# Kernel optimization log

Measured on AMD Instinct MI355X. Metric: run time of the kernel, lower is better.

The kernel has to match this reference:

```python
import jax, jax.numpy as jnp
import numpy as np

C = 64           # channels
CPG = 8          # channel_per_group
G = C // CPG     # offset groups = 8
K = 27           # 3x3x3 taps
N, D, H, W = 2, 8, 56, 56


def conv3d(x, w, b=None):
    y = jax.lax.conv_general_dilated(
        x, w, window_strides=(1, 1, 1), padding=[(1, 1)] * 3,
        dimension_numbers=('NCDHW', 'OIDHW', 'NCDHW'))
    if b is not None:
        y = y + b.reshape(1, -1, 1, 1, 1)
    return y


def deform_conv3d(x, off, w, groups):
    # x: [N,C,D,H,W]; off: [N, G*3*27, D,H,W]; w: [O,C,3,3,3]
    n, cin, d, h, wd = x.shape
    cpg = cin // groups
    p = d * h * wd
    off = off.reshape(n, groups, K, 3, d, h, wd)
    # kernel tap displacements in (kd,kh,kw) order, each in {-1,0,1}
    r = jnp.arange(3, dtype=x.dtype) - 1.0
    taps = jnp.stack(jnp.meshgrid(r, r, r, indexing='ij'), axis=-1).reshape(K, 3)
    gd = jnp.arange(d, dtype=x.dtype)[:, None, None]
    gh = jnp.arange(h, dtype=x.dtype)[None, :, None]
    gw = jnp.arange(wd, dtype=x.dtype)[None, None, :]
    # sampling positions [N,G,K,D,H,W]
    pd = gd + taps[:, 0][:, None, None, None] + off[:, :, :, 0]
    ph = gh + taps[:, 1][:, None, None, None] + off[:, :, :, 1]
    pw = gw + taps[:, 2][:, None, None, None] + off[:, :, :, 2]
    d0 = jnp.floor(pd); h0 = jnp.floor(ph); w0 = jnp.floor(pw)
    fd, fh, fw = pd - d0, ph - h0, pw - w0
    d0 = d0.astype(jnp.int32); h0 = h0.astype(jnp.int32); w0 = w0.astype(jnp.int32)
    xflat = x.reshape(n, groups, cpg, p)[:, :, None]  # [N,G,1,Cpg,P]
    acc = jnp.zeros((n, groups, K, cpg, p), x.dtype)
    for cd in (0, 1):
        for ch in (0, 1):
            for cw in (0, 1):
                idd, idh, idw = d0 + cd, h0 + ch, w0 + cw
                wgt = ((fd if cd else 1.0 - fd)
                       * (fh if ch else 1.0 - fh)
                       * (fw if cw else 1.0 - fw))
                valid = ((idd >= 0) & (idd < d) & (idh >= 0) & (idh < h)
                         & (idw >= 0) & (idw < wd)).astype(x.dtype)
                lin = ((jnp.clip(idd, 0, d - 1) * h + jnp.clip(idh, 0, h - 1)) * wd
                       + jnp.clip(idw, 0, wd - 1))
                g = jnp.take_along_axis(xflat, lin.reshape(n, groups, K, 1, p), axis=-1)
                acc = acc + g * (wgt * valid).reshape(n, groups, K, 1, p)
    # [N,G,K,Cpg,P] -> [N,K,C,P]
    vals = acc.transpose(0, 2, 1, 3, 4).reshape(n, K, cin, p)
    out = jnp.einsum('oik,nkip->nop', w.reshape(w.shape[0], cin, K), vals)
    return out.reshape(n, -1, d, h, wd)


def batchnorm(x, gamma, beta, eps=1e-5):
    m = x.mean((0, 2, 3, 4), keepdims=True)
    v = x.var((0, 2, 3, 4), keepdims=True)
    return (gamma.reshape(1, -1, 1, 1, 1) * (x - m) * jax.lax.rsqrt(v + eps)
            + beta.reshape(1, -1, 1, 1, 1))


def setup_inputs() -> dict:
    key = jax.random.key(0)
    ks = jax.random.split(key, 4)
    fan = C * K
    x = jax.random.normal(ks[0], (N, C, D, H, W), jnp.float32)
    w_off = jax.random.normal(ks[1], (G * 3 * K, C, 3, 3, 3), jnp.float32) * 0.01
    b_off = jnp.zeros((G * 3 * K,), jnp.float32)
    w1 = jax.random.normal(ks[2], (C, C, 3, 3, 3), jnp.float32) / np.sqrt(fan).astype(np.float32)
    w2 = jax.random.normal(ks[3], (C, C, 3, 3, 3), jnp.float32) / np.sqrt(fan).astype(np.float32)
    return dict(x=x, w_off=w_off, b_off=b_off, w1=w1,
                gamma1=jnp.ones((C,), jnp.float32), beta1=jnp.zeros((C,), jnp.float32),
                w2=w2, b2=jnp.zeros((C,), jnp.float32),
                gamma2=jnp.ones((C,), jnp.float32), beta2=jnp.zeros((C,), jnp.float32))


def reference(x, w_off, b_off, w1, gamma1, beta1, w2, b2, gamma2, beta2):
    residual = x
    off = conv3d(x, w_off, b_off)
    out = deform_conv3d(x, off, w1, G)
    out = jax.nn.relu(batchnorm(out, gamma1, beta1))
    out = conv3d(out, w2, b2)
    out = batchnorm(out, gamma2, beta2) + residual
    return jax.nn.relu(out)
```

## Files before the change

### kernel.cpp

```cpp
#include <hip/hip_runtime.h>
#include <hip/hip_bf16.h>

#define N_ 2
#define C_ 64
#define D_ 8
#define H_ 56
#define W_ 56
#define HW_ (H_*W_)
#define P_ (D_*HW_)
#define G_ 8
#define CPG_ 8
#define K_ 27
#define CO_OFF_ 648
#define MP_ 768
#define KK_ 1728
#define KB_ (KK_*2)

typedef __attribute__((ext_vector_type(8))) short shortx8;
typedef __attribute__((ext_vector_type(4))) float floatx4;
#define AS1 __attribute__((address_space(1)))
#define AS3 __attribute__((address_space(3)))

__device__ inline float b2f(unsigned short u) {
    union { unsigned u; float f; } x; x.u = ((unsigned)u) << 16; return x.f;
}
__device__ inline unsigned short f2b(float f) {
    union { float f; unsigned u; } x; x.f = f;
    unsigned r = (x.u + 0x7fffu + ((x.u >> 16) & 1u)) >> 16;
    return (unsigned short)r;
}
__device__ inline float lof(unsigned u) { union { unsigned u; float f; } x; x.u = u << 16; return x.f; }
__device__ inline float hif(unsigned u) { union { unsigned u; float f; } x; x.u = u & 0xffff0000u; return x.f; }
__device__ inline unsigned cvt_pk_bf16(float a, float b) {
    unsigned r;
    asm("v_cvt_pk_bf16_f32 %0, %1, %2" : "=v"(r) : "v"(a), "v"(b));
    return r;
}


__global__ __launch_bounds__(256) void transpose_xt_kernel(
    const float* __restrict__ x, unsigned short* __restrict__ xt)
{
    __shared__ unsigned short tile[64][65];
    int b  = blockIdx.x;
    int n  = b / (P_/64);
    int p0 = (b % (P_/64))*64;
    int tid = threadIdx.x;
    int j  = tid & 63;
    int c0 = (tid >> 6)*16;
    for (int r = 0; r < 16; ++r)
        tile[c0 + r][j] = f2b(x[((size_t)n*C_ + c0 + r)*P_ + p0 + j]);
    __syncthreads();
    unsigned* dst = (unsigned*)(xt + ((size_t)n*P_ + p0)*C_);
    #pragma unroll
    for (int it = 0; it < 8; ++it) {
        int wi  = it*256 + tid;
        int row = wi >> 5;
        int c   = (wi & 31)*2;
        unsigned lo = tile[c][row], hi = tile[c+1][row];
        dst[(size_t)row*32 + (wi & 31)] = lo | (hi << 16);
    }
}

__global__ __launch_bounds__(256) void permA1k_kernel(
    const float* __restrict__ w, unsigned short* __restrict__ A)
{
    int i = blockIdx.x*256 + threadIdx.x;
    if (i >= MP_*KK_) return;
    int m = i / KK_, r = i % KK_;
    int kk = r / 64, ci = r % 64;
    A[i] = (m < CO_OFF_) ? f2b(w[((size_t)m*C_ + ci)*K_ + kk]) : (unsigned short)0;
}

__global__ __launch_bounds__(256) void perm_w_kernel(
    const float* __restrict__ w, unsigned short* __restrict__ At)
{
    int tid = blockIdx.x*256 + threadIdx.x;
    if (tid >= C_*KK_) return;
    int o  = tid / KK_;
    int r  = tid % KK_;
    int k  = r / 64, i = r % 64;
    At[tid] = f2b(w[((size_t)o*C_ + i)*K_ + k]);
}

__global__ __launch_bounds__(256, 2) void conv_off_fused(
    const unsigned short* __restrict__ A,
    const unsigned short* __restrict__ xt,
    const float* __restrict__ bias,
    unsigned short* __restrict__ off2)
{
    __shared__ __align__(16) short As[2][16*512];
    __shared__ __align__(16) short Bs[32*512];
    int tid = threadIdx.x;
    int w = tid >> 6, lane = tid & 63;
    int n   = blockIdx.x / 490;
    int bid = blockIdx.x % 490;
    int mt = bid / 98, nt = bid % 98;
    int m0 = mt*128, p0 = nt*256;
    int lm = lane & 15, lq = lane >> 4;

    const unsigned short* xtn = xt + (size_t)n*P_*C_;
    unsigned short* out2 = off2 + (size_t)n*216*P_*3;

    const char* Ab0 = (const char*)A + (size_t)(m0 + w*32 + lm)*KB_ + lq*16;
    const char* Ab1 = Ab0 + (size_t)16*KB_;

    int oct = lane & 7;
    int prj[8], dj[8], hj[8], wj[8];
    #pragma unroll
    for (int j = 0; j < 8; ++j) {
        int prow = j*32 + w*8 + (lane >> 3);
        prj[j] = prow;
        int p = p0 + prow;
        dj[j] = p / HW_;
        int hw2 = p % HW_;
        hj[j] = hw2 / W_;
        wj[j] = hw2 % W_;
    }

    auto stageA = [&](int kt, int buf) {
        __builtin_amdgcn_global_load_lds((const AS1 unsigned*)(Ab0 + kt*128),      (AS3 unsigned*)(&As[buf][(w*2)*512]),     16, 0, 0);
        __builtin_amdgcn_global_load_lds((const AS1 unsigned*)(Ab1 + kt*128),      (AS3 unsigned*)(&As[buf][(w*2+1)*512]),   16, 0, 0);
        __builtin_amdgcn_global_load_lds((const AS1 unsigned*)(Ab0 + kt*128 + 64), (AS3 unsigned*)(&As[buf][(8+w*2)*512]),   16, 0, 0);
        __builtin_amdgcn_global_load_lds((const AS1 unsigned*)(Ab1 + kt*128 + 64), (AS3 unsigned*)(&As[buf][(8+w*2+1)*512]), 16, 0, 0);
    };
    auto loadB = [&](int kt, uint4* B) {
        int kd = kt/9 - 1, kh = (kt/3)%3 - 1, kw = kt%3 - 1;
        int delta = kd*HW_ + kh*W_ + kw;
        #pragma unroll
        for (int j = 0; j < 8; ++j) {
            bool v = ((unsigned)(dj[j]+kd) < (unsigned)D_) &&
                     ((unsigned)(hj[j]+kh) < (unsigned)H_) &&
                     ((unsigned)(wj[j]+kw) < (unsigned)W_);
            uint4 val = {0u,0u,0u,0u};
            if (v) val = *(const uint4*)(xtn + (size_t)(p0 + prj[j] + delta)*C_ + oct*8);
            B[j] = val;
        }
    };

    int mh = w >> 1, nh = w & 1;
    floatx4 acc[4][8];
    #pragma unroll
    for (int i = 0; i < 4; ++i)
        #pragma unroll
        for (int j = 0; j < 8; ++j)
            acc[i][j] = (floatx4){0.f, 0.f, 0.f, 0.f};

    uint4 Bcur[8], Bnext[8];
    #pragma unroll
    for (int j = 0; j < 8; ++j) Bnext[j] = (uint4){0u,0u,0u,0u};
    stageA(0, 0);
    loadB(0, Bcur);

    for (int kt = 0; kt < 27; ++kt) {
        int buf = kt & 1;
        __syncthreads();
        #pragma unroll
        for (int j = 0; j < 8; ++j) {
            int chunk = (oct>>2)*16 + (prj[j]>>4);
            *(uint4*)&Bs[chunk*512 + ((oct&3)*16 + ((prj[j]&15) ^ oct))*8] = Bcur[j];
        }
        __syncthreads();
        if (kt < 26) { stageA(kt+1, buf^1); loadB(kt+1, Bnext); }
        #pragma unroll
        for (int ks = 0; ks < 2; ++ks) {
            int swzB = (lq*16 + (lm ^ (ks*4 + lq)))*8;
            shortx8 a[4];
            #pragma unroll
            for (int i = 0; i < 4; ++i) a[i] = *(const shortx8*)&As[buf][(ks*8 + 4*mh + i)*512 + lane*8];
            #pragma unroll
            for (int j = 0; j < 8; ++j) {
                shortx8 b = *(const shortx8*)&Bs[(ks*16 + 8*nh + j)*512 + swzB];
                #pragma unroll
                for (int i = 0; i < 4; ++i)
                    acc[i][j] = __builtin_amdgcn_mfma_f32_16x16x32_bf16(a[i], b, acc[i][j], 0, 0, 0);
            }
        }
        #pragma unroll
        for (int j = 0; j < 8; ++j) Bcur[j] = Bnext[j];
    }

    #pragma unroll
    for (int i = 0; i < 4; ++i) {
        int cob = m0 + (4*mh+i)*16 + lq*4;
        #pragma unroll
        for (int r = 0; r < 4; ++r) {
            int co = cob + r;
            float bv = bias[co];
            int row2 = co / 3, comp = co % 3;
            size_t base = (size_t)row2*P_*3 + comp;
            #pragma unroll
            for (int j = 0; j < 8; ++j) {
                int col = p0 + (8*nh+j)*16 + lm;
                out2[base + (size_t)col*3] = f2b(acc[i][j][r] + bv);
            }
        }
    }
}

__global__ __launch_bounds__(256) void conv_off_tail(
    const unsigned short* __restrict__ A,
    const unsigned short* __restrict__ xt,
    const float* __restrict__ bias,
    unsigned short* __restrict__ off2)
{
    __shared__ __align__(16) short As[54*512];
    __shared__ __align__(16) short Bs[16*512];
    int tid = threadIdx.x;
    int w = tid >> 6, lane = tid & 63;
    int n  = blockIdx.x / 196;
    int p0 = (blockIdx.x % 196)*128;
    int lm = lane & 15, lq = lane >> 4;

    const unsigned short* xtn = xt + (size_t)n*P_*C_;
    unsigned short* out2 = off2 + (size_t)n*216*P_*3;

    const char* Abase = (const char*)A + (size_t)(640 + lm)*KB_ + lq*16;
    for (int ch = w; ch < 54; ch += 4)
        __builtin_amdgcn_global_load_lds((const AS1 unsigned*)(Abase + ch*64),
                                         (AS3 unsigned*)(As + ch*512), 16, 0, 0);

    int oct = lane & 7;
    int prj[4], dj[4], hj[4], wj[4];
    #pragma unroll
    for (int j = 0; j < 4; ++j) {
        int prow = j*32 + w*8 + (lane >> 3);
        prj[j] = prow;
        int p = p0 + prow;
        dj[j] = p / HW_;
        int hw2 = p % HW_;
        hj[j] = hw2 / W_;
        wj[j] = hw2 % W_;
    }
    auto loadB = [&](int kt, uint4* B) {
        int kd = kt/9 - 1, kh = (kt/3)%3 - 1, kw = kt%3 - 1;
        int delta = kd*HW_ + kh*W_ + kw;
        #pragma unroll
        for (int j = 0; j < 4; ++j) {
            bool v = ((unsigned)(dj[j]+kd) < (unsigned)D_) &&
                     ((unsigned)(hj[j]+kh) < (unsigned)H_) &&
                     ((unsigned)(wj[j]+kw) < (unsigned)W_);
            uint4 val = {0u,0u,0u,0u};
            if (v) val = *(const uint4*)(xtn + (size_t)(p0 + prj[j] + delta)*C_ + oct*8);
            B[j] = val;
        }
    };

    floatx4 acc[2];
    acc[0] = (floatx4){0.f,0.f,0.f,0.f};
    acc[1] = (floatx4){0.f,0.f,0.f,0.f};

    uint4 Bcur[4], Bnext[4];
    #pragma unroll
    for (int j = 0; j < 4; ++j) Bnext[j] = (uint4){0u,0u,0u,0u};
    loadB(0, Bcur);

    for (int kt = 0; kt < 27; ++kt) {
        __syncthreads();
        #pragma unroll
        for (int j = 0; j < 4; ++j) {
            int chunk = (oct>>2)*8 + (prj[j]>>4);
            *(uint4*)&Bs[chunk*512 + ((oct&3)*16 + ((prj[j]&15) ^ oct))*8] = Bcur[j];
        }
        __syncthreads();
        if (kt < 26) loadB(kt+1, Bnext);
        #pragma unroll
        for (int ks = 0; ks < 2; ++ks) {
            int swzB = (lq*16 + (lm ^ (ks*4 + lq)))*8;
            shortx8 a = *(const shortx8*)&As[(kt*2 + ks)*512 + lane*8];
            #pragma unroll
            for (int j = 0; j < 2; ++j) {
                shortx8 b = *(const shortx8*)&Bs[(ks*8 + w*2 + j)*512 + swzB];
                acc[j] = __builtin_amdgcn_mfma_f32_16x16x32_bf16(a, b, acc[j], 0, 0, 0);
            }
        }
        #pragma unroll
        for (int j = 0; j < 4; ++j) Bcur[j] = Bnext[j];
    }

    #pragma unroll
    for (int j = 0; j < 2; ++j) {
        #pragma unroll
        for (int r = 0; r < 4; ++r) {
            int co = 640 + lq*4 + r;
            if (co < CO_OFF_) {
                int col = p0 + w*32 + j*16 + lm;
                out2[((size_t)(co/3)*P_ + col)*3 + (co%3)] = f2b(acc[j][r] + bias[co]);
            }
        }
    }
}

__global__ __launch_bounds__(256) void deform_fused(
    const unsigned short* __restrict__ xt,
    const unsigned short* __restrict__ off2,
    const unsigned short* __restrict__ A,
    unsigned short* __restrict__ y1t)
{
    __shared__ __align__(16) short SH[12288];
    int tid = threadIdx.x;
    int w = tid >> 6, lane = tid & 63;
    int n  = blockIdx.x / (P_/32);
    int p0 = (blockIdx.x % (P_/32))*32;
    int lm = lane & 15, lq = lane >> 4;

    const unsigned short* offn = off2 + (size_t)n*216*P_*3;
    const uint4* xg0 = (const uint4*)(xt + (size_t)n*P_*C_);

    const char* Ab = (const char*)A + (size_t)(w*16 + lm)*KB_ + lq*16;

    int g = lane & 7;
    int prow = tid >> 3;
    int p = p0 + prow;
    int dd = p / HW_;
    int hw2 = p % HW_;
    int hh = hw2 / W_;
    int ww = hw2 % W_;
    int bchunk = (g>>2)*2 + (prow>>4);
    int boffs  = ((g&3)*16 + ((prow&15) ^ g))*8;

    auto stageA = [&](int kt, int buf) {
        __builtin_amdgcn_global_load_lds((const AS1 unsigned*)(Ab + kt*128),      (AS3 unsigned*)(SH + buf*4096 + w*512),     16, 0, 0);
        __builtin_amdgcn_global_load_lds((const AS1 unsigned*)(Ab + kt*128 + 64), (AS3 unsigned*)(SH + buf*4096 + (4+w)*512), 16, 0, 0);
    };
    auto loadOff = [&](int kt, float* o) {
        size_t idx = ((size_t)(g*K_ + kt)*P_ + p)*3;
        o[0] = b2f(offn[idx]);
        o[1] = b2f(offn[idx + 1]);
        o[2] = b2f(offn[idx + 2]);
    };
    auto issueCorners = [&](int kt, float* o, uint4* V, float* Wt) {
        int kd = kt/9 - 1, kh = (kt/3)%3 - 1, kw = kt%3 - 1;
        float pd = (float)(dd + kd) + o[0];
        float ph = (float)(hh + kh) + o[1];
        float pw = (float)(ww + kw) + o[2];
        float fd0 = floorf(pd), fh0 = floorf(ph), fw0 = floorf(pw);
        int d0 = (int)fd0, h0 = (int)fh0, w0i = (int)fw0;
        float fd = pd - fd0, fh = ph - fh0, fw = pw - fw0;
        int dc0 = min(max(d0, 0), D_-1),   dc1 = min(max(d0+1, 0), D_-1);
        int hc0 = min(max(h0, 0), H_-1),   hc1 = min(max(h0+1, 0), H_-1);
        int wc0 = min(max(w0i, 0), W_-1),  wc1 = min(max(w0i+1, 0), W_-1);
        float wd0 = ((unsigned)d0      < (unsigned)D_) ? 1.f - fd : 0.f;
        float wd1 = ((unsigned)(d0+1)  < (unsigned)D_) ? fd       : 0.f;
        float wh0 = ((unsigned)h0      < (unsigned)H_) ? 1.f - fh : 0.f;
        float wh1 = ((unsigned)(h0+1)  < (unsigned)H_) ? fh       : 0.f;
        float ww0 = ((unsigned)w0i     < (unsigned)W_) ? 1.f - fw : 0.f;
        float ww1 = ((unsigned)(w0i+1) < (unsigned)W_) ? fw       : 0.f;
        int rb00 = (dc0*H_ + hc0)*W_, rb01 = (dc0*H_ + hc1)*W_;
        int rb10 = (dc1*H_ + hc0)*W_, rb11 = (dc1*H_ + hc1)*W_;
        float wdh00 = wd0*wh0, wdh01 = wd0*wh1, wdh10 = wd1*wh0, wdh11 = wd1*wh1;
        V[0] = xg0[(size_t)(rb00+wc0)*8 + g];  Wt[0] = wdh00*ww0;
        V[1] = xg0[(size_t)(rb00+wc1)*8 + g];  Wt[1] = wdh00*ww1;
        V[2] = xg0[(size_t)(rb01+wc0)*8 + g];  Wt[2] = wdh01*ww0;
        V[3] = xg0[(size_t)(rb01+wc1)*8 + g];  Wt[3] = wdh01*ww1;
        V[4] = xg0[(size_t)(rb10+wc0)*8 + g];  Wt[4] = wdh10*ww0;
        V[5] = xg0[(size_t)(rb10+wc1)*8 + g];  Wt[5] = wdh10*ww1;
        V[6] = xg0[(size_t)(rb11+wc0)*8 + g];  Wt[6] = wdh11*ww0;
        V[7] = xg0[(size_t)(rb11+wc1)*8 + g];  Wt[7] = wdh11*ww1;
    };
    auto reduceCorners = [&](uint4* V, float* Wt, uint4& o4) {
        float res[CPG_];
        #pragma unroll
        for (int c = 0; c < CPG_; ++c) res[c] = 0.f;
        #pragma unroll
        for (int c = 0; c < 8; ++c) {
            uint4 v4 = V[c];
            float wgt = Wt[c];
            res[0] = fmaf(wgt, lof(v4.x), res[0]);
            res[1] = fmaf(wgt, hif(v4.x), res[1]);
            res[2] = fmaf(wgt, lof(v4.y), res[2]);
            res[3] = fmaf(wgt, hif(v4.y), res[3]);
            res[4] = fmaf(wgt, lof(v4.z), res[4]);
            res[5] = fmaf(wgt, hif(v4.z), res[5]);
            res[6] = fmaf(wgt, lof(v4.w), res[6]);
            res[7] = fmaf(wgt, hif(v4.w), res[7]);
        }
        o4.x = cvt_pk_bf16(res[0], res[1]);
        o4.y = cvt_pk_bf16(res[2], res[3]);
        o4.z = cvt_pk_bf16(res[4], res[5]);
        o4.w = cvt_pk_bf16(res[6], res[7]);
    };

    int mh = w >> 1, nh = w & 1;
    floatx4 acc[2];
    acc[0] = (floatx4){0.f,0.f,0.f,0.f};
    acc[1] = (floatx4){0.f,0.f,0.f,0.f};

    float offA[3], offB[3], offT[3];
    uint4 Vv[8]; float Wt[8];
    uint4 o4cur;

    stageA(0, 0);
    loadOff(0, offA);
    loadOff(1, offB);
    issueCorners(0, offA, Vv, Wt);
    reduceCorners(Vv, Wt, o4cur);
    *(uint4*)&SH[8192 + bchunk*512 + boffs] = o4cur;

    for (int kt = 0; kt < 27; ++kt) {
        int buf = kt & 1;
        __syncthreads();
        if (kt < 26) {
            stageA(kt+1, buf^1);
            if (kt < 25) loadOff(kt+2, offT);
            issueCorners(kt+1, offB, Vv, Wt);
        }
        #pragma unroll
        for (int ks = 0; ks < 2; ++ks) {
            int swzB = (lq*16 + (lm ^ (ks*4 + lq)))*8;
            shortx8 b = *(const shortx8*)&SH[8192 + buf*2048 + (ks*2 + nh)*512 + swzB];
            #pragma unroll
            for (int i = 0; i < 2; ++i) {
                shortx8 a = *(const shortx8*)&SH[buf*4096 + (ks*4 + 2*mh+i)*512 + lane*8];
                acc[i] = __builtin_amdgcn_mfma_f32_16x16x32_bf16(a, b, acc[i], 0, 0, 0);
            }
        }
        if (kt < 26) {
            reduceCorners(Vv, Wt, o4cur);
            *(uint4*)&SH[8192 + (buf^1)*2048 + bchunk*512 + boffs] = o4cur;
            offB[0] = offT[0]; offB[1] = offT[1]; offB[2] = offT[2];
        }
    }

    __syncthreads();
    #pragma unroll
    for (int i = 0; i < 2; ++i) {
        int ob = mh*32 + i*16 + lq*4;
        int pc = nh*16 + lm;
        #pragma unroll
        for (int rr = 0; rr < 4; ++rr)
            SH[pc*72 + ob + rr] = (short)f2b(acc[i][rr]);
    }
    __syncthreads();
    {
        int row = tid >> 3, seg = tid & 7;
        uint4 v = *(const uint4*)&SH[row*72 + seg*8];
        *(uint4*)(y1t + ((size_t)n*P_ + p0 + row)*C_ + seg*8) = v;
    }
}

__global__ __launch_bounds__(256) void conv2_fused(
    const unsigned short* __restrict__ y1t,
    const float* __restrict__ st1,
    const unsigned short* __restrict__ A,
    const float* __restrict__ bias,
    unsigned short* __restrict__ y2)
{
    __shared__ __align__(16) short As[4][4096];
    __shared__ float sc[64], sf[64];
    int tid = threadIdx.x;
    if (tid < 64) sc[tid] = st1[tid];
    else if (tid < 128) sf[tid-64] = st1[tid];
    int w = tid >> 6, lane = tid & 63;
    int n  = blockIdx.x / (P_/64);
    int p0 = (blockIdx.x % (P_/64))*64;
    int lm = lane & 15, lq = lane >> 4;

    const unsigned short* y1n = y1t + (size_t)n*P_*C_;
    unsigned short* y2n = y2 + (size_t)n*C_*P_;
    const char* Ab = (const char*)A + (size_t)(w*16 + lm)*KB_ + lq*16;

    int p = p0 + w*16 + lm;
    int dd = p / HW_, hw2 = p % HW_;
    int hh = hw2 / W_, ww = hw2 % W_;

    auto stageA = [&](int kt) {
        int buf = kt & 3;
        __builtin_amdgcn_global_load_lds((const AS1 unsigned*)(Ab + kt*128),      (AS3 unsigned*)(&As[buf][w*512]),     16, 0, 0);
        __builtin_amdgcn_global_load_lds((const AS1 unsigned*)(Ab + kt*128 + 64), (AS3 unsigned*)(&As[buf][(4+w)*512]), 16, 0, 0);
    };
    auto issueV = [&](int kt, uint4* V, int& M) {
        int kd = kt/9 - 1, kh = (kt/3)%3 - 1, kw = kt%3 - 1;
        int delta = kd*HW_ + kh*W_ + kw;
        bool v = ((unsigned)(dd+kd) < (unsigned)D_) &&
                 ((unsigned)(hh+kh) < (unsigned)H_) &&
                 ((unsigned)(ww+kw) < (unsigned)W_);
        M = v ? 1 : 0;
        #pragma unroll
        for (int ks = 0; ks < 2; ++ks) {
            uint4 val = {0u,0u,0u,0u};
            if (v) val = *(const uint4*)(y1n + (size_t)(p + delta)*C_ + (ks*4 + lq)*8);
            V[ks] = val;
        }
    };
    auto reduceT = [&](uint4 V, int ks, int M) -> shortx8 {
        uint4 o4 = {0u,0u,0u,0u};
        if (M) {
            int cb = (ks*4 + lq)*8;
            float r0 = fmaxf(lof(V.x)*sc[cb+0] + sf[cb+0], 0.f);
            float r1 = fmaxf(hif(V.x)*sc[cb+1] + sf[cb+1], 0.f);
            float r2 = fmaxf(lof(V.y)*sc[cb+2] + sf[cb+2], 0.f);
            float r3 = fmaxf(hif(V.y)*sc[cb+3] + sf[cb+3], 0.f);
            float r4 = fmaxf(lof(V.z)*sc[cb+4] + sf[cb+4], 0.f);
            float r5 = fmaxf(hif(V.z)*sc[cb+5] + sf[cb+5], 0.f);
            float r6 = fmaxf(lof(V.w)*sc[cb+6] + sf[cb+6], 0.f);
            float r7 = fmaxf(hif(V.w)*sc[cb+7] + sf[cb+7], 0.f);
            o4.x = cvt_pk_bf16(r0, r1);
            o4.y = cvt_pk_bf16(r2, r3);
            o4.z = cvt_pk_bf16(r4, r5);
            o4.w = cvt_pk_bf16(r6, r7);
        }
        return *(shortx8*)&o4;
    };

    floatx4 acc[4];
    #pragma unroll
    for (int i = 0; i < 4; ++i) acc[i] = (floatx4){0.f,0.f,0.f,0.f};

    auto mfmaTap = [&](int kt, shortx8 b0, shortx8 b1) {
        int buf = kt & 3;
        #pragma unroll
        for (int i = 0; i < 4; ++i) {
            shortx8 a = *(const shortx8*)&As[buf][(0*4 + i)*512 + lane*8];
            acc[i] = __builtin_amdgcn_mfma_f32_16x16x32_bf16(a, b0, acc[i], 0, 0, 0);
        }
        #pragma unroll
        for (int i = 0; i < 4; ++i) {
            shortx8 a = *(const shortx8*)&As[buf][(1*4 + i)*512 + lane*8];
            acc[i] = __builtin_amdgcn_mfma_f32_16x16x32_bf16(a, b1, acc[i], 0, 0, 0);
        }
    };

    uint4 VA[2], VB[2];
    int MA, MB;
    stageA(0); stageA(1);
    issueV(0, VA, MA);
    issueV(1, VB, MB);

    for (int kt = 0; kt < 26; kt += 2) {
        __syncthreads();
        stageA(kt+2);
        if (kt+3 <= 26) stageA(kt+3);
        {
            shortx8 b0 = reduceT(VA[0], 0, MA);
            shortx8 b1 = reduceT(VA[1], 1, MA);
            issueV(kt+2, VA, MA);
            mfmaTap(kt, b0, b1);
        }
        {
            shortx8 b0 = reduceT(VB[0], 0, MB);
            shortx8 b1 = reduceT(VB[1], 1, MB);
            if (kt+3 <= 26) issueV(kt+3, VB, MB);
            mfmaTap(kt+1, b0, b1);
        }
    }
    __syncthreads();
    {
        shortx8 b0 = reduceT(VA[0], 0, MA);
        shortx8 b1 = reduceT(VA[1], 1, MA);
        mfmaTap(26, b0, b1);
    }

    #pragma unroll
    for (int i = 0; i < 4; ++i) {
        #pragma unroll
        for (int r = 0; r < 4; ++r) {
            int co = i*16 + lq*4 + r;
            y2n[(size_t)co*P_ + p] = f2b(acc[i][r] + bias[co]);
        }
    }
}

__global__ __launch_bounds__(256) void stats_partial_kernel(
    const unsigned short* __restrict__ y1t, float* __restrict__ part)
{
    int b = blockIdx.x, tid = threadIdx.x;
    int c = tid & 63, sub = tid >> 6;
    float s = 0.f, q = 0.f;
    for (int rr = 0; rr < 128; ++rr) {
        int row = b*512 + sub*128 + rr;
        float v = b2f(y1t[(size_t)row*C_ + c]);
        s += v;
        q = fmaf(v, v, q);
    }
    __shared__ float ss[256], qq[256];
    ss[tid] = s; qq[tid] = q;
    __syncthreads();
    if (tid < 64) {
        float S = ss[tid] + ss[64+tid] + ss[128+tid] + ss[192+tid];
        float Q = qq[tid] + qq[64+tid] + qq[128+tid] + qq[192+tid];
        part[b*128 + tid]      = S;
        part[b*128 + 64 + tid] = Q;
    }
}

__global__ void stats_final_kernel(
    const float* __restrict__ part,
    const float* __restrict__ gamma, const float* __restrict__ beta,
    float* __restrict__ st1)
{
    int c = threadIdx.x;
    float S = 0.f, Q = 0.f;
    for (int b = 0; b < 98; ++b) {
        S += part[b*128 + c];
        Q += part[b*128 + 64 + c];
    }
    const float inv = 1.f / (float)(N_*P_);
    float m = S * inv;
    float var = Q * inv - m*m;
    float scale = rsqrtf(var + 1e-5f) * gamma[c];
    st1[c]      = scale;
    st1[64 + c] = beta[c] - m*scale;
}

__global__ __launch_bounds__(256) void bn_stats_kernel(
    const unsigned short* __restrict__ src, float* __restrict__ stats)
{
    int c   = blockIdx.x;
    int tid = threadIdx.x;
    float s = 0.f, q = 0.f;
    for (int n = 0; n < N_; ++n) {
        const unsigned short* p = src + ((size_t)n*C_ + c)*P_;
        for (int i = tid; i < P_; i += 256) {
            float v = b2f(p[i]);
            s += v;
            q = fmaf(v, v, q);
        }
    }
    #pragma unroll
    for (int o = 32; o; o >>= 1) {
        s += __shfl_down(s, o);
        q += __shfl_down(q, o);
    }
    __shared__ float sh[2][4];
    int wave = tid >> 6;
    if ((tid & 63) == 0) { sh[0][wave] = s; sh[1][wave] = q; }
    __syncthreads();
    if (tid == 0) {
        float S = sh[0][0] + sh[0][1] + sh[0][2] + sh[0][3];
        float Q = sh[1][0] + sh[1][1] + sh[1][2] + sh[1][3];
        const float inv = 1.f / (float)(N_*P_);
        float m  = S * inv;
        float var = Q * inv - m*m;
        stats[c]      = m;
        stats[C_ + c] = rsqrtf(var + 1e-5f);
    }
}

__global__ __launch_bounds__(256) void bn_add_relu_kernel(
    const unsigned short* __restrict__ y2, const float* __restrict__ x,
    const float* __restrict__ stats,
    const float* __restrict__ gamma, const float* __restrict__ beta,
    float* __restrict__ out)
{
    size_t idx = (size_t)blockIdx.x*256 + threadIdx.x;
    int c = (int)((idx / P_) % C_);
    float v = (b2f(y2[idx]) - stats[c]) * stats[C_ + c] * gamma[c] + beta[c] + x[idx];
    out[idx] = fmaxf(v, 0.f);
}

extern "C" void kernel_launch(void* const* d_in, const int* in_sizes, int n_in,
                              void* d_out, int out_size, void* d_ws, size_t ws_size,
                              hipStream_t stream) {
    const float* x     = (const float*)d_in[0];
    const float* w_off = (const float*)d_in[1];
    const float* b_off = (const float*)d_in[2];
    const float* w1    = (const float*)d_in[3];
    const float* g1    = (const float*)d_in[4];
    const float* be1   = (const float*)d_in[5];
    const float* w2    = (const float*)d_in[6];
    const float* b2    = (const float*)d_in[7];
    const float* g2    = (const float*)d_in[8];
    const float* be2   = (const float*)d_in[9];
    float* out = (float*)d_out;

    float* st1  = (float*)d_ws;
    float* st2  = st1 + 128;
    float* part = st2 + 128;
    unsigned short* off2 = (unsigned short*)(part + 98*128);
    unsigned short* xt  = off2 + (size_t)N_*216*P_*3;
    unsigned short* y1t = xt  + (size_t)N_*P_*C_;
    unsigned short* y2  = y1t + (size_t)N_*P_*C_;
    unsigned short* A1k = y2  + (size_t)N_*C_*P_;
    unsigned short* A1t = A1k + (size_t)MP_*KK_;
    unsigned short* A2t = A1t + (size_t)C_*KK_;

    transpose_xt_kernel<<<N_*(P_/64), 256, 0, stream>>>(x, xt);
    permA1k_kernel<<<(MP_*KK_+255)/256, 256, 0, stream>>>(w_off, A1k);
    perm_w_kernel<<<(C_*KK_+255)/256, 256, 0, stream>>>(w1, A1t);
    perm_w_kernel<<<(C_*KK_+255)/256, 256, 0, stream>>>(w2, A2t);

    conv_off_fused<<<2*490, 256, 0, stream>>>(A1k, xt, b_off, off2);
    conv_off_tail<<<2*196, 256, 0, stream>>>(A1k, xt, b_off, off2);

    deform_fused<<<N_*(P_/32), 256, 0, stream>>>(xt, off2, A1t, y1t);

    stats_partial_kernel<<<98, 256, 0, stream>>>(y1t, part);
    stats_final_kernel<<<1, 64, 0, stream>>>(part, g1, be1, st1);

    conv2_fused<<<N_*(P_/64), 256, 0, stream>>>(y1t, st1, A2t, b2, y2);

    bn_stats_kernel<<<C_, 256, 0, stream>>>(y2, st2);
    bn_add_relu_kernel<<<(N_*C_*P_)/256, 256, 0, stream>>>(y2, x, st2, g2, be2, out);
}
```

Baseline: 519.9 us.

## Merge offset-conv tail into main kernel, fuse BN2 stats into conv2, vectorize epilogue

The offset-conv tail blocks are folded into the main offset-conv launch through a block-index branch over a shared LDS buffer, removing one launch and the serialization between them. Conv2 now reduces per-channel sum and sum-of-squares in its epilogue and writes per-block partials, which replaces the separate stats pass over y2 with a small final reduction kernel. The BN+add+ReLU kernel is vectorized to process four elements per thread with a precomputed scale and shift. The partials reuse the off2 buffer, which is dead by that point, and the larger LDS footprint of the merged kernel may reduce occupancy.

After: 467.0 us. -10.2%, faster.

```diff
diff --git a/kernel.cpp b/kernel.cpp
--- a/kernel.cpp
+++ b/kernel.cpp
@@ -89,203 +89,198 @@
     const float* __restrict__ bias,
     unsigned short* __restrict__ off2)
 {
-    __shared__ __align__(16) short As[2][16*512];
-    __shared__ __align__(16) short Bs[32*512];
+    __shared__ __align__(16) short SH[35840];
     int tid = threadIdx.x;
     int w = tid >> 6, lane = tid & 63;
-    int n   = blockIdx.x / 490;
-    int bid = blockIdx.x % 490;
-    int mt = bid / 98, nt = bid % 98;
-    int m0 = mt*128, p0 = nt*256;
     int lm = lane & 15, lq = lane >> 4;
 
-    const unsigned short* xtn = xt + (size_t)n*P_*C_;
-    unsigned short* out2 = off2 + (size_t)n*216*P_*3;
-
-    const char* Ab0 = (const char*)A + (size_t)(m0 + w*32 + lm)*KB_ + lq*16;
-    const char* Ab1 = Ab0 + (size_t)16*KB_;
-
-    int oct = lane & 7;
-    int prj[8], dj[8], hj[8], wj[8];
-    #pragma unroll
-    for (int j = 0; j < 8; ++j) {
-        int prow = j*32 + w*8 + (lane >> 3);
-        prj[j] = prow;
-        int p = p0 + prow;
-        dj[j] = p / HW_;
-        int hw2 = p % HW_;
-        hj[j] = hw2 / W_;
-        wj[j] = hw2 % W_;
-    }
-
-    auto stageA = [&](int kt, int buf) {
-        __builtin_amdgcn_global_load_lds((const AS1 unsigned*)(Ab0 + kt*128),      (AS3 unsigned*)(&As[buf][(w*2)*512]),     16, 0, 0);
-        __builtin_amdgcn_global_load_lds((const AS1 unsigned*)(Ab1 + kt*128),      (AS3 unsigned*)(&As[buf][(w*2+1)*512]),   16, 0, 0);
-        __builtin_amdgcn_global_load_lds((const AS1 unsigned*)(Ab0 + kt*128 + 64), (AS3 unsigned*)(&As[buf][(8+w*2)*512]),   16, 0, 0);
-        __builtin_amdgcn_global_load_lds((const AS1 unsigned*)(Ab1 + kt*128 + 64), (AS3 unsigned*)(&As[buf][(8+w*2+1)*512]), 16, 0, 0);
-    };
-    auto loadB = [&](int kt, uint4* B) {
-        int kd = kt/9 - 1, kh = (kt/3)%3 - 1, kw = kt%3 - 1;
-        int delta = kd*HW_ + kh*W_ + kw;
+    if (blockIdx.x < 2*490) {
+        short* As0 = SH;
+        short* Bs  = SH + 2*16*512;
+        int n   = blockIdx.x / 490;
+        int bid = blockIdx.x % 490;
+        int mt = bid / 98, nt = bid % 98;
+        int m0 = mt*128, p0 = nt*256;
+
+        const unsigned short* xtn = xt + (size_t)n*P_*C_;
+        unsigned short* out2 = off2 + (size_t)n*216*P_*3;
+
+        const char* Ab0 = (const char*)A + (size_t)(m0 + w*32 + lm)*KB_ + lq*16;
+        const char* Ab1 = Ab0 + (size_t)16*KB_;
+
+        int oct = lane & 7;
+        int prj[8], dj[8], hj[8], wj[8];
         #pragma unroll
         for (int j = 0; j < 8; ++j) {
-            bool v = ((unsigned)(dj[j]+kd) < (unsigned)D_) &&
-                     ((unsigned)(hj[j]+kh) < (unsigned)H_) &&
-                     ((unsigned)(wj[j]+kw) < (unsigned)W_);
-            uint4 val = {0u,0u,0u,0u};
-            if (v) val = *(const uint4*)(xtn + (size_t)(p0 + prj[j] + delta)*C_ + oct*8);
-            B[j] = val;
-        }
-    };
-
-    int mh = w >> 1, nh = w & 1;
-    floatx4 acc[4][8];
-    #pragma unroll
-    for (int i = 0; i < 4; ++i)
-        #pragma unroll
-        for (int j = 0; j < 8; ++j)
-            acc[i][j] = (floatx4){0.f, 0.f, 0.f, 0.f};
-
-    uint4 Bcur[8], Bnext[8];
-    #pragma unroll
-    for (int j = 0; j < 8; ++j) Bnext[j] = (uint4){0u,0u,0u,0u};
-    stageA(0, 0);
-    loadB(0, Bcur);
-
-    for (int kt = 0; kt < 27; ++kt) {
-        int buf = kt & 1;
-        __syncthreads();
-        #pragma unroll
-        for (int j = 0; j < 8; ++j) {
-            int chunk = (oct>>2)*16 + (prj[j]>>4);
-            *(uint4*)&Bs[chunk*512 + ((oct&3)*16 + ((prj[j]&15) ^ oct))*8] = Bcur[j];
-        }
-        __syncthreads();
-        if (kt < 26) { stageA(kt+1, buf^1); loadB(kt+1, Bnext); }
-        #pragma unroll
-        for (int ks = 0; ks < 2; ++ks) {
-            int swzB = (lq*16 + (lm ^ (ks*4 + lq)))*8;
-            shortx8 a[4];
-            #pragma unroll
-            for (int i = 0; i < 4; ++i) a[i] = *(const shortx8*)&As[buf][(ks*8 + 4*mh + i)*512 + lane*8];
+            int prow = j*32 + w*8 + (lane >> 3);
+            prj[j] = prow;
+            int p = p0 + prow;
+            dj[j] = p / HW_;
+            int hw2 = p % HW_;
+            hj[j] = hw2 / W_;
+            wj[j] = hw2 % W_;
+        }
+
+        auto stageA = [&](int kt, int buf) {
+            __builtin_amdgcn_global_load_lds((const AS1 unsigned*)(Ab0 + kt*128),      (AS3 unsigned*)(As0 + buf*8192 + (w*2)*512),     16, 0, 0);
+            __builtin_amdgcn_global_load_lds((const AS1 unsigned*)(Ab1 + kt*128),      (AS3 unsigned*)(As0 + buf*8192 + (w*2+1)*512),   16, 0, 0);
+            __builtin_amdgcn_global_load_lds((const AS1 unsigned*)(Ab0 + kt*128 + 64), (AS3 unsigned*)(As0 + buf*8192 + (8+w*2)*512),   16, 0, 0);
+            __builtin_amdgcn_global_load_lds((const AS1 unsigned*)(Ab1 + kt*128 + 64), (AS3 unsigned*)(As0 + buf*8192 + (8+w*2+1)*512), 16, 0, 0);
+        };
+        auto loadB = [&](int kt, uint4* B) {
+            int kd = kt/9 - 1, kh = (kt/3)%3 - 1, kw = kt%3 - 1;
+            int delta = kd*HW_ + kh*W_ + kw;
             #pragma unroll
             for (int j = 0; j < 8; ++j) {
-                shortx8 b = *(const shortx8*)&Bs[(ks*16 + 8*nh + j)*512 + swzB];
+                bool v = ((unsigned)(dj[j]+kd) < (unsigned)D_) &&
+                         ((unsigned)(hj[j]+kh) < (unsigned)H_) &&
+                         ((unsigned)(wj[j]+kw) < (unsigned)W_);
+                uint4 val = {0u,0u,0u,0u};
+                if (v) val = *(const uint4*)(xtn + (size_t)(p0 + prj[j] + delta)*C_ + oct*8);
+                B[j] = val;
+            }
+        };
+
+        int mh = w >> 1, nh = w & 1;
+        floatx4 acc[4][8];
+        #pragma unroll
+        for (int i = 0; i < 4; ++i)
+            #pragma unroll
+            for (int j = 0; j < 8; ++j)
+                acc[i][j] = (floatx4){0.f, 0.f, 0.f, 0.f};
+
+        uint4 Bcur[8], Bnext[8];
+        #pragma unroll
+        for (int j = 0; j < 8; ++j) Bnext[j] = (uint4){0u,0u,0u,0u};
+        stageA(0, 0);
+        loadB(0, Bcur);
+
+        for (int kt = 0; kt < 27; ++kt) {
+            int buf = kt & 1;
+            __syncthreads();
+            #pragma unroll
+            for (int j = 0; j < 8; ++j) {
+                int chunk = (oct>>2)*16 + (prj[j]>>4);
+                *(uint4*)&Bs[chunk*512 + ((oct&3)*16 + ((prj[j]&15) ^ oct))*8] = Bcur[j];
+            }
+            __syncthreads();
+            if (kt < 26) { stageA(kt+1, buf^1); loadB(kt+1, Bnext); }
+            #pragma unroll
+            for (int ks = 0; ks < 2; ++ks) {
+                int swzB = (lq*16 + (lm ^ (ks*4 + lq)))*8;
+                shortx8 a[4];
                 #pragma unroll
-                for (int i = 0; i < 4; ++i)
-                    acc[i][j] = __builtin_amdgcn_mfma_f32_16x16x32_bf16(a[i], b, acc[i][j], 0, 0, 0);
-            }
-        }
-        #pragma unroll
-        for (int j = 0; j < 8; ++j) Bcur[j] = Bnext[j];
-    }
-
-    #pragma unroll
-    for (int i = 0; i < 4; ++i) {
-        int cob = m0 + (4*mh+i)*16 + lq*4;
-        #pragma unroll
-        for (int r = 0; r < 4; ++r) {
-            int co = cob + r;
-            float bv = bias[co];
-            int row2 = co / 3, comp = co % 3;
-            size_t base = (size_t)row2*P_*3 + comp;
-            #pragma unroll
-            for (int j = 0; j < 8; ++j) {
-                int col = p0 + (8*nh+j)*16 + lm;
-                out2[base + (size_t)col*3] = f2b(acc[i][j][r] + bv);
-            }
-        }
-    }
-}
-
-__global__ __launch_bounds__(256) void conv_off_tail(
-    const unsigned short* __restrict__ A,
-    const unsigned short* __restrict__ xt,
-    const float* __restrict__ bias,
-    unsigned short* __restrict__ off2)
-{
-    __shared__ __align__(16) short As[54*512];
-    __shared__ __align__(16) short Bs[16*512];
-    int tid = threadIdx.x;
-    int w = tid >> 6, lane = tid & 63;
-    int n  = blockIdx.x / 196;
-    int p0 = (blockIdx.x % 196)*128;
-    int lm = lane & 15, lq = lane >> 4;
-
-    const unsigned short* xtn = xt + (size_t)n*P_*C_;
-    unsigned short* out2 = off2 + (size_t)n*216*P_*3;
-
-    const char* Abase = (const char*)A + (size_t)(640 + lm)*KB_ + lq*16;
-    for (int ch = w; ch < 54; ch += 4)
-        __builtin_amdgcn_global_load_lds((const AS1 unsigned*)(Abase + ch*64),
-                                         (AS3 unsigned*)(As + ch*512), 16, 0, 0);
-
-    int oct = lane & 7;
-    int prj[4], dj[4], hj[4], wj[4];
-    #pragma unroll
-    for (int j = 0; j < 4; ++j) {
-        int prow = j*32 + w*8 + (lane >> 3);
-        prj[j] = prow;
-        int p = p0 + prow;
-        dj[j] = p / HW_;
-        int hw2 = p % HW_;
-        hj[j] = hw2 / W_;
-        wj[j] = hw2 % W_;
-    }
-    auto loadB = [&](int kt, uint4* B) {
-        int kd = kt/9 - 1, kh = (kt/3)%3 - 1, kw = kt%3 - 1;
-        int delta = kd*HW_ + kh*W_ + kw;
+                for (int i = 0; i < 4; ++i) a[i] = *(const shortx8*)&As0[buf*8192 + (ks*8 + 4*mh + i)*512 + lane*8];
+                #pragma unroll
+                for (int j = 0; j < 8; ++j) {
+                    shortx8 b = *(const shortx8*)&Bs[(ks*16 + 8*nh + j)*512 + swzB];
+                    #pragma unroll
+                    for (int i = 0; i < 4; ++i)
+                        acc[i][j] = __builtin_amdgcn_mfma_f32_16x16x32_bf16(a[i], b, acc[i][j], 0, 0, 0);
+                }
+            }
+            #pragma unroll
+            for (int j = 0; j < 8; ++j) Bcur[j] = Bnext[j];
+        }
+
+        #pragma unroll
+        for (int i = 0; i < 4; ++i) {
+            int cob = m0 + (4*mh+i)*16 + lq*4;
+            #pragma unroll
+            for (int r = 0; r < 4; ++r) {
+                int co = cob + r;
+                float bv = bias[co];
+                int row2 = co / 3, comp = co % 3;
+                size_t base = (size_t)row2*P_*3 + comp;
+                #pragma unroll
+                for (int j = 0; j < 8; ++j) {
+                    int col = p0 + (8*nh+j)*16 + lm;
+                    out2[base + (size_t)col*3] = f2b(acc[i][j][r] + bv);
+                }
+            }
+        }
+    } else {
+        short* As = SH;
+        short* Bs = SH + 54*512;
+        int t  = blockIdx.x - 2*490;
+        int n  = t / 196;
+        int p0 = (t % 196)*128;
+
+        const unsigned short* xtn = xt + (size_t)n*P_*C_;
+        unsigned short* out2 = off2 + (size_t)n*216*P_*3;
+
+        const char* Abase = (const char*)A + (size_t)(640 + lm)*KB_ + lq*16;
+        for (int ch = w; ch < 54; ch += 4)
+            __builtin_amdgcn_global_load_lds((const AS1 unsigned*)(Abase + ch*64),
+                                             (AS3 unsigned*)(As + ch*512), 16, 0, 0);
+
+        int oct = lane & 7;
+        int prj[4], dj[4], hj[4], wj[4];
         #pragma unroll
         for (int j = 0; j < 4; ++j) {
-            bool v = ((unsigned)(dj[j]+kd) < (unsigned)D_) &&
-                     ((unsigned)(hj[j]+kh) < (unsigned)H_) &&
-                     ((unsigned)(wj[j]+kw) < (unsigned)W_);
-            uint4 val = {0u,0u,0u,0u};
-            if (v) val = *(const uint4*)(xtn + (size_t)(p0 + prj[j] + delta)*C_ + oct*8);
-            B[j] = val;
-        }
-    };
-
-    floatx4 acc[2];
-    acc[0] = (floatx4){0.f,0.f,0.f,0.f};
-    acc[1] = (floatx4){0.f,0.f,0.f,0.f};
-
-    uint4 Bcur[4], Bnext[4];
-    #pragma unroll
-    for (int j = 0; j < 4; ++j) Bnext[j] = (uint4){0u,0u,0u,0u};
-    loadB(0, Bcur);
-
-    for (int kt = 0; kt < 27; ++kt) {
-        __syncthreads();
-        #pragma unroll
-        for (int j = 0; j < 4; ++j) {
-            int chunk = (oct>>2)*8 + (prj[j]>>4);
-            *(uint4*)&Bs[chunk*512 + ((oct&3)*16 + ((prj[j]&15) ^ oct))*8] = Bcur[j];
-        }
-        __syncthreads();
-        if (kt < 26) loadB(kt+1, Bnext);
-        #pragma unroll
-        for (int ks = 0; ks < 2; ++ks) {
-            int swzB = (lq*16 + (lm ^ (ks*4 + lq)))*8;
-            shortx8 a = *(const shortx8*)&As[(kt*2 + ks)*512 + lane*8];
-            #pragma unroll
-            for (int j = 0; j < 2; ++j) {
-                shortx8 b = *(const shortx8*)&Bs[(ks*8 + w*2 + j)*512 + swzB];
-                acc[j] = __builtin_amdgcn_mfma_f32_16x16x32_bf16(a, b, acc[j], 0, 0, 0);
-            }
-        }
-        #pragma unroll
-        for (int j = 0; j < 4; ++j) Bcur[j] = Bnext[j];
-    }
-
-    #pragma unroll
-    for (int j = 0; j < 2; ++j) {
-        #pragma unroll
-        for (int r = 0; r < 4; ++r) {
-            int co = 640 + lq*4 + r;
-            if (co < CO_OFF_) {
-                int col = p0 + w*32 + j*16 + lm;
-                out2[((size_t)(co/3)*P_ + col)*3 + (co%3)] = f2b(acc[j][r] + bias[co]);
+            int prow = j*32 + w*8 + (lane >> 3);
+            prj[j] = prow;
+            int p = p0 + prow;
+            dj[j] = p / HW_;
+            int hw2 = p % HW_;
+            hj[j] = hw2 / W_;
+            wj[j] = hw2 % W_;
+        }
+        auto loadB = [&](int kt, uint4* B) {
+            int kd = kt/9 - 1, kh = (kt/3)%3 - 1, kw = kt%3 - 1;
+            int delta = kd*HW_ + kh*W_ + kw;
+            #pragma unroll
+            for (int j = 0; j < 4; ++j) {
+                bool v = ((unsigned)(dj[j]+kd) < (unsigned)D_) &&
+                         ((unsigned)(hj[j]+kh) < (unsigned)H_) &&
+                         ((unsigned)(wj[j]+kw) < (unsigned)W_);
+                uint4 val = {0u,0u,0u,0u};
+                if (v) val = *(const uint4*)(xtn + (size_t)(p0 + prj[j] + delta)*C_ + oct*8);
+                B[j] = val;
+            }
+        };
+
+        floatx4 acc[2];
+        acc[0] = (floatx4){0.f,0.f,0.f,0.f};
+        acc[1] = (floatx4){0.f,0.f,0.f,0.f};
+
+        uint4 Bcur[4], Bnext[4];
+        #pragma unroll
+        for (int j = 0; j < 4; ++j) Bnext[j] = (uint4){0u,0u,0u,0u};
+        loadB(0, Bcur);
+
+        for (int kt = 0; kt < 27; ++kt) {
+            __syncthreads();
+            #pragma unroll
+            for (int j = 0; j < 4; ++j) {
+                int chunk = (oct>>2)*8 + (prj[j]>>4);
+                *(uint4*)&Bs[chunk*512 + ((oct&3)*16 + ((prj[j]&15) ^ oct))*8] = Bcur[j];
+            }
+            __syncthreads();
+            if (kt < 26) loadB(kt+1, Bnext);
+            #pragma unroll
+            for (int ks = 0; ks < 2; ++ks) {
+                int swzB = (lq*16 + (lm ^ (ks*4 + lq)))*8;
+                shortx8 a = *(const shortx8*)&As[(kt*2 + ks)*512 + lane*8];
+                #pragma unroll
+                for (int j = 0; j < 2; ++j) {
+                    shortx8 b = *(const shortx8*)&Bs[(ks*8 + w*2 + j)*512 + swzB];
+                    acc[j] = __builtin_amdgcn_mfma_f32_16x16x32_bf16(a, b, acc[j], 0, 0, 0);
+                }
+            }
+            #pragma unroll
+            for (int j = 0; j < 4; ++j) Bcur[j] = Bnext[j];
+        }
+
+        #pragma unroll
+        for (int j = 0; j < 2; ++j) {
+            #pragma unroll
+            for (int r = 0; r < 4; ++r) {
+                int co = 640 + lq*4 + r;
+                if (co < CO_OFF_) {
+                    int col = p0 + w*32 + j*16 + lm;
+                    out2[((size_t)(co/3)*P_ + col)*3 + (co%3)] = f2b(acc[j][r] + bias[co]);
+                }
             }
         }
     }
@@ -444,10 +439,12 @@
     const float* __restrict__ st1,
     const unsigned short* __restrict__ A,
     const float* __restrict__ bias,
-    unsigned short* __restrict__ y2)
+    unsigned short* __restrict__ y2,
+    float* __restrict__ part2)
 {
     __shared__ __align__(16) short As[4][4096];
     __shared__ float sc[64], sf[64];
+    __shared__ float SP[4][64], SQ[4][64];
     int tid = threadIdx.x;
     if (tid < 64) sc[tid] = st1[tid];
     else if (tid < 128) sf[tid-64] = st1[tid];
@@ -556,8 +553,23 @@
         #pragma unroll
         for (int r = 0; r < 4; ++r) {
             int co = i*16 + lq*4 + r;
-            y2n[(size_t)co*P_ + p] = f2b(acc[i][r] + bias[co]);
-        }
+            float v = acc[i][r] + bias[co];
+            y2n[(size_t)co*P_ + p] = f2b(v);
+            float s = v, q = v*v;
+            #pragma unroll
+            for (int m = 1; m < 16; m <<= 1) {
+                s += __shfl_xor(s, m);
+                q += __shfl_xor(q, m);
+            }
+            if (lm == 0) { SP[w][co] = s; SQ[w][co] = q; }
+        }
+    }
+    __syncthreads();
+    if (tid < 64) {
+        float S = SP[0][tid] + SP[1][tid] + SP[2][tid] + SP[3][tid];
+        float Q = SQ[0][tid] + SQ[1][tid] + SQ[2][tid] + SQ[3][tid];
+        part2[(size_t)blockIdx.x*128 + tid]      = S;
+        part2[(size_t)blockIdx.x*128 + 64 + tid] = Q;
     }
 }
 
@@ -603,50 +615,48 @@
     st1[64 + c] = beta[c] - m*scale;
 }
 
-__global__ __launch_bounds__(256) void bn_stats_kernel(
-    const unsigned short* __restrict__ src, float* __restrict__ stats)
-{
-    int c   = blockIdx.x;
+__global__ __launch_bounds__(256) void bn2_final_kernel(
+    const float* __restrict__ part2,
+    const float* __restrict__ gamma, const float* __restrict__ beta,
+    float* __restrict__ st2)
+{
     int tid = threadIdx.x;
-    float s = 0.f, q = 0.f;
-    for (int n = 0; n < N_; ++n) {
-        const unsigned short* p = src + ((size_t)n*C_ + c)*P_;
-        for (int i = tid; i < P_; i += 256) {
-            float v = b2f(p[i]);
-            s += v;
-            q = fmaf(v, v, q);
-        }
-    }
-    #pragma unroll
-    for (int o = 32; o; o >>= 1) {
-        s += __shfl_down(s, o);
-        q += __shfl_down(q, o);
-    }
-    __shared__ float sh[2][4];
-    int wave = tid >> 6;
-    if ((tid & 63) == 0) { sh[0][wave] = s; sh[1][wave] = q; }
+    int c = tid & 63, seg = tid >> 6;
+    float S = 0.f, Q = 0.f;
+    for (int b = seg*196; b < seg*196 + 196; ++b) {
+        S += part2[(size_t)b*128 + c];
+        Q += part2[(size_t)b*128 + 64 + c];
+    }
+    __shared__ float ss[256], qq[256];
+    ss[tid] = S; qq[tid] = Q;
     __syncthreads();
-    if (tid == 0) {
-        float S = sh[0][0] + sh[0][1] + sh[0][2] + sh[0][3];
-        float Q = sh[1][0] + sh[1][1] + sh[1][2] + sh[1][3];
+    if (tid < 64) {
+        float St = ss[tid] + ss[64+tid] + ss[128+tid] + ss[192+tid];
+        float Qt = qq[tid] + qq[64+tid] + qq[128+tid] + qq[192+tid];
         const float inv = 1.f / (float)(N_*P_);
-        float m  = S * inv;
-        float var = Q * inv - m*m;
-        stats[c]      = m;
-        stats[C_ + c] = rsqrtf(var + 1e-5f);
+        float m = St * inv;
+        float var = Qt * inv - m*m;
+        float scale = rsqrtf(var + 1e-5f) * gamma[tid];
+        st2[tid]      = scale;
+        st2[64 + tid] = beta[tid] - m*scale;
     }
 }
 
 __global__ __launch_bounds__(256) void bn_add_relu_kernel(
     const unsigned short* __restrict__ y2, const float* __restrict__ x,
-    const float* __restrict__ stats,
-    const float* __restrict__ gamma, const float* __restrict__ beta,
-    float* __restrict__ out)
-{
-    size_t idx = (size_t)blockIdx.x*256 + threadIdx.x;
-    int c = (int)((idx / P_) % C_);
-    float v = (b2f(y2[idx]) - stats[c]) * stats[C_ + c] * gamma[c] + beta[c] + x[idx];
-    out[idx] = fmaxf(v, 0.f);
+    const float* __restrict__ st2, float* __restrict__ out)
+{
+    size_t i4 = ((size_t)blockIdx.x*256 + threadIdx.x)*4;
+    int c = (int)((i4 / P_) % C_);
+    float scale = st2[c], shift = st2[64 + c];
+    uint2 yv = *(const uint2*)(y2 + i4);
+    float4 xv = *(const float4*)(x + i4);
+    float4 o;
+    o.x = fmaxf(fmaf(lof(yv.x), scale, shift) + xv.x, 0.f);
+    o.y = fmaxf(fmaf(hif(yv.x), scale, shift) + xv.y, 0.f);
+    o.z = fmaxf(fmaf(lof(yv.y), scale, shift) + xv.z, 0.f);
+    o.w = fmaxf(fmaf(hif(yv.y), scale, shift) + xv.w, 0.f);
+    *(float4*)(out + i4) = o;
 }
 
 extern "C" void kernel_launch(void* const* d_in, const int* in_sizes, int n_in,
@@ -674,22 +684,22 @@
     unsigned short* A1k = y2  + (size_t)N_*C_*P_;
     unsigned short* A1t = A1k + (size_t)MP_*KK_;
     unsigned short* A2t = A1t + (size_t)C_*KK_;
+    float* part2 = (float*)off2;
 
     transpose_xt_kernel<<<N_*(P_/64), 256, 0, stream>>>(x, xt);
     permA1k_kernel<<<(MP_*KK_+255)/256, 256, 0, stream>>>(w_off, A1k);
     perm_w_kernel<<<(C_*KK_+255)/256, 256, 0, stream>>>(w1, A1t);
     perm_w_kernel<<<(C_*KK_+255)/256, 256, 0, stream>>>(w2, A2t);
 
-    conv_off_fused<<<2*490, 256, 0, stream>>>(A1k, xt, b_off, off2);
-    conv_off_tail<<<2*196, 256, 0, stream>>>(A1k, xt, b_off, off2);
+    conv_off_fused<<<2*490 + 2*196, 256, 0, stream>>>(A1k, xt, b_off, off2);
 
     deform_fused<<<N_*(P_/32), 256, 0, stream>>>(xt, off2, A1t, y1t);
 
     stats_partial_kernel<<<98, 256, 0, stream>>>(y1t, part);
     stats_final_kernel<<<1, 64, 0, stream>>>(part, g1, be1, st1);
 
-    conv2_fused<<<N_*(P_/64), 256, 0, stream>>>(y1t, st1, A2t, b2, y2);
-
-    bn_stats_kernel<<<C_, 256, 0, stream>>>(y2, st2);
-    bn_add_relu_kernel<<<(N_*C_*P_)/256, 256, 0, stream>>>(y2, x, st2, g2, be2, out);
-}
+    conv2_fused<<<N_*(P_/64), 256, 0, stream>>>(y1t, st1, A2t, b2, y2, part2);
+
+    bn2_final_kernel<<<1, 256, 0, stream>>>(part2, g2, be2, st2);
+    bn_add_relu_kernel<<<(N_*C_*P_)/1024, 256, 0, stream>>>(y2, x, st2, out);
+}
```
